# Performance work log

Hardware: AMD Instinct MI355X
Metric: run time of the kernel (lower is better)

The kernel has to match this reference:

```python
import jax, jax.numpy as jnp
import numpy as np

D_MODEL = 1024
NUM_HEADS = 16
HEAD_DIM = D_MODEL // NUM_HEADS


def setup_inputs() -> dict:
    key = jax.random.key(0)
    ks = jax.random.split(key, 5)
    s = 1.0 / np.sqrt(D_MODEL)
    return {
        "x": jax.random.normal(ks[0], (2, 2048, D_MODEL), dtype=jnp.float32),
        "Wqkv": jax.random.normal(ks[1], (3 * D_MODEL, D_MODEL), dtype=jnp.float32) * s,
        "bqkv": jax.random.normal(ks[2], (3 * D_MODEL,), dtype=jnp.float32) * s,
        "Wo": jax.random.normal(ks[3], (D_MODEL, D_MODEL), dtype=jnp.float32) * s,
        "bo": jax.random.normal(ks[4], (D_MODEL,), dtype=jnp.float32) * s,
    }


def reference(x, Wqkv, bqkv, Wo, bo):
    B, S, D = x.shape
    H, hd = NUM_HEADS, HEAD_DIM
    # fused QKV projection (torch Linear: x @ W.T + b)
    qkv = x @ Wqkv.T + bqkv                      # [B, S, 3D]
    qkv = qkv.reshape(B, S, H, 3 * hd).transpose(0, 2, 1, 3)  # [B, H, S, 3hd]
    q, k, v = jnp.split(qkv, 3, axis=-1)         # each [B, H, S, hd]
    scaled = jnp.einsum("bhqd,bhkd->bhqk", q, k) / jnp.sqrt(jnp.float32(hd))
    # module applies causal mask when its `mask` flag is False (the default)
    causal = jnp.tril(jnp.ones((S, S), dtype=bool))
    scaled = jnp.where(causal, scaled, -jnp.inf)
    attn = jax.nn.softmax(scaled, axis=-1)       # [B, H, S, S]
    values = jnp.einsum("bhqk,bhkd->bhqd", attn, v)  # [B, H, S, hd]
    # NOTE: original uses .reshape (not transpose-then-reshape) on the
    # [B, H, S, hd] tensor directly — reproduce that exact layout.
    values = values.reshape(B, S, H * hd)
    out = values @ Wo.T + bo                     # [B, S, D]
    return out
```

## Files before the change

### kernel.cpp

```cpp
#include <hip/hip_runtime.h>

typedef __attribute__((ext_vector_type(8))) short bf16x8;
typedef __attribute__((ext_vector_type(4))) float f32x4;

#define D_MODEL 1024
#define NHEADS 16
#define HDIM 64
#define SEQ 2048
#define BATCH 2
#define MROWS (BATCH*SEQ)
#define NQKV (3*D_MODEL)
#define QSCALE 0.1803368801111204f
#define CSTR 144

__device__ __forceinline__ unsigned short f2bf(float f) {
  unsigned int u = __float_as_uint(f);
  u += 0x7FFF + ((u >> 16) & 1);
  return (unsigned short)(u >> 16);
}
__device__ __forceinline__ unsigned int pack2bf(float a, float b) {
#if __has_builtin(__builtin_amdgcn_cvt_pk_bf16_f32)
  auto r = __builtin_amdgcn_cvt_pk_bf16_f32(a, b);
  unsigned int u; __builtin_memcpy(&u, &r, 4);
  return u;
#else
  return ((unsigned int)f2bf(b) << 16) | (unsigned int)f2bf(a);
#endif
}

__device__ __forceinline__ void gload16(const void* g, void* l) {
  __builtin_amdgcn_global_load_lds((const __attribute__((address_space(1))) void*)g,
                                   (__attribute__((address_space(3))) void*)l, 16, 0, 0);
}

#define N4_X     1048576
#define N4_WQKV   786432
#define N4_WO     262144
__global__ void cvt_all_kernel(const float4* __restrict__ x,
                               const float4* __restrict__ wqkv,
                               const float4* __restrict__ wo,
                               ushort4* __restrict__ xb,
                               ushort4* __restrict__ wqkvb,
                               ushort4* __restrict__ wob) {
  int i = blockIdx.x * blockDim.x + threadIdx.x;
  const float4* s; ushort4* d; int j;
  if (i < N4_X)                { s = x;    d = xb;    j = i; }
  else if (i < N4_X + N4_WQKV) { s = wqkv; d = wqkvb; j = i - N4_X; }
  else                         { s = wo;   d = wob;   j = i - (N4_X + N4_WQKV); }
  float4 v = s[j];
  ushort4 o;
  o.x = f2bf(v.x); o.y = f2bf(v.y); o.z = f2bf(v.z); o.w = f2bf(v.w);
  d[j] = o;
}

template<int MODE, int BM>
__global__ __launch_bounds__(256) void gemm_bt_kernel(
    const unsigned short* __restrict__ A,
    const unsigned short* __restrict__ Bm,
    const float* __restrict__ bias,
    float* __restrict__ outF,
    unsigned short* __restrict__ Qb,
    unsigned short* __restrict__ Kb,
    unsigned short* __restrict__ VTb,
    int M, int N, int K)
{
  constexpr int MI = BM / 32;
  constexpr int STG = BM*32 + 128*32;
  constexpr int SHSZ = (MODE == 0 && 128*CSTR > 2*STG) ? 128*CSTR : 2*STG;
  __shared__ __align__(16) unsigned short Sh[SHSZ];
  const int tid = threadIdx.x;
  const int wave = tid >> 6, lane = tid & 63;
  const int lm = lane & 15, quad = lane >> 4;
  const int wm = (wave >> 1) * (BM/2), wn = (wave & 1) * 64;
  const int m0 = blockIdx.y * BM, n0 = blockIdx.x * 128;

  f32x4 acc[MI][4] = {};

  auto stage_in = [&](int k0, int sb) {
    unsigned short* As = Sh + sb*STG;
    unsigned short* Bs = As + BM*32;
#pragma unroll
    for (int i = 0; i < BM/64; i++) {
      int ch = i*256 + tid;
      int r = ch >> 2, cg = (ch & 3) ^ ((r >> 1) & 3);
      gload16(&A[(size_t)(m0 + r) * K + k0 + cg*8], &As[ch*8]);
    }
#pragma unroll
    for (int i = 0; i < 2; i++) {
      int ch = i*256 + tid;
      int r = ch >> 2, cg = (ch & 3) ^ ((r >> 1) & 3);
      gload16(&Bm[(size_t)(n0 + r) * K + k0 + cg*8], &Bs[ch*8]);
    }
  };

  stage_in(0, 0);
  for (int k0 = 0; k0 < K; k0 += 32) {
    const int cur = (k0 >> 5) & 1;
    __syncthreads();
    if (k0 + 32 < K) stage_in(k0 + 32, cur ^ 1);
    const unsigned short* As = Sh + cur*STG;
    const unsigned short* Bs = As + BM*32;
    bf16x8 af[MI], bfr[4];
#pragma unroll
    for (int mi = 0; mi < MI; mi++) {
      int r = wm + mi*16 + lm;
      af[mi] = *(const bf16x8*)&As[(r*4 + (quad ^ ((r >> 1) & 3))) * 8];
    }
#pragma unroll
    for (int ni = 0; ni < 4; ni++) {
      int r = wn + ni*16 + lm;
      bfr[ni] = *(const bf16x8*)&Bs[(r*4 + (quad ^ ((r >> 1) & 3))) * 8];
    }
#pragma unroll
    for (int mi = 0; mi < MI; mi++)
#pragma unroll
      for (int ni = 0; ni < 4; ni++)
        acc[mi][ni] = __builtin_amdgcn_mfma_f32_16x16x32_bf16(af[mi], bfr[ni], acc[mi][ni], 0, 0, 0);
  }

  if (MODE == 1) {
#pragma unroll
    for (int mi = 0; mi < MI; mi++)
#pragma unroll
      for (int ni = 0; ni < 4; ni++)
#pragma unroll
        for (int r = 0; r < 4; r++) {
          int row = m0 + wm + mi*16 + quad*4 + r;
          int col = n0 + wn + ni*16 + lm;
          outF[(size_t)row * N + col] = acc[mi][ni][r] + bias[col];
        }
  } else {
    __syncthreads();
#pragma unroll
    for (int mi = 0; mi < MI; mi++)
#pragma unroll
      for (int ni = 0; ni < 4; ni++)
#pragma unroll
        for (int r = 0; r < 4; r++) {
          int row_l = wm + mi*16 + quad*4 + r;
          int col_l = wn + ni*16 + lm;
          int col = n0 + col_l;
          float v = acc[mi][ni][r] + bias[col];
          if (((col % 192) >> 6) == 0) v *= QSCALE;
          Sh[row_l*CSTR + col_l] = f2bf(v);
        }
    __syncthreads();
#pragma unroll
    for (int i = 0; i < 8; i++) {
      int lin = i*256 + tid;
      int row_l = lin >> 4, cc = (lin & 15) * 8;
      int col = n0 + cc;
      int h = col / 192, rr = col - h*192;
      int ty = rr >> 6, e = rr & 63;
      if (ty < 2) {
        uint4 d = *(const uint4*)&Sh[row_l*CSTR + cc];
        int row = m0 + row_l;
        int b = row >> 11, s = row & (SEQ - 1);
        unsigned short* dst = ty ? Kb : Qb;
        *(uint4*)&dst[((size_t)(b*NHEADS + h)*SEQ + s)*HDIM + e] = d;
      }
    }
#pragma unroll
    for (int i = 0; i < 8; i++) {
      int lin = i*256 + tid;
      int col_l = lin & 127, s8 = (lin >> 7) * 8;
      int col = n0 + col_l;
      int h = col / 192, rr = col - h*192;
      if ((rr >> 6) == 2) {
        int e = rr & 63;
        unsigned short tmp[8];
#pragma unroll
        for (int j = 0; j < 8; j++) tmp[j] = Sh[(s8 + j)*CSTR + col_l];
        int row = m0 + s8;
        int b = row >> 11, s = row & (SEQ - 1);
        size_t vb = ((size_t)(b*NHEADS + h)*HDIM + e)*SEQ;
        int pos = (s & ~31) | (((s >> 2) & 3) << 3) | (((s >> 4) & 1) << 2);
        *(uint2*)&VTb[vb + pos]     = *(const uint2*)&tmp[0];
        *(uint2*)&VTb[vb + pos + 8] = *(const uint2*)&tmp[4];
      }
    }
  }
}

__global__ __launch_bounds__(256) void flash_attn_kernel(
    const unsigned short* __restrict__ Qb,
    const unsigned short* __restrict__ Kb,
    const unsigned short* __restrict__ VTb,
    unsigned short* __restrict__ Ob)
{
  const int tid = threadIdx.x;
  const int wave = tid >> 6, lane = tid & 63;
  const int lm = lane & 15, quad = lane >> 4;
  const int bx = blockIdx.x;
  const int bh = (bx & 7) * 4 + (bx >> 3);
  const int pr = blockIdx.y;
  const int t0 = 31 - pr, t1 = pr;
  const int nk0 = (t0 + 2) >> 1;
  const int ntot = nk0 + ((t1 + 2) >> 1);

  __shared__ __align__(16) unsigned short Ks[2][128*64];
  __shared__ __align__(16) unsigned short Vs[2][64*128];

  const unsigned short* Qbh  = Qb  + (size_t)bh*SEQ*HDIM;
  const unsigned short* Kbh  = Kb  + (size_t)bh*SEQ*HDIM;
  const unsigned short* VTbh = VTb + (size_t)bh*HDIM*SEQ;

  auto stage_in = [&](int k0, int sb) {
#pragma unroll
    for (int i = 0; i < 4; i++) {
      int ch = i*256 + tid;
      int r = ch >> 3, cg = (ch & 7) ^ (r & 7);
      gload16(&Kbh[(size_t)(k0 + r)*HDIM + cg*8], &Ks[sb][ch*8]);
    }
#pragma unroll
    for (int i = 0; i < 4; i++) {
      int ch = i*256 + tid;
      int e = ch >> 4, cg = (ch & 15) ^ (e & 7);
      gload16(&VTbh[(size_t)e*SEQ + k0 + cg*8], &Vs[sb][ch*8]);
    }
  };

  int rowq = t0*64 + wave*16;
  int query = rowq + lm;
  bf16x8 qf[2];
#pragma unroll
  for (int kc = 0; kc < 2; kc++)
    qf[kc] = *(const bf16x8*)&Qbh[(size_t)query*HDIM + kc*32 + quad*8];

  f32x4 o[4] = {};
  float m_run = -1e30f, l_run = 0.f;

  stage_in(0, 0);
  for (int s = 0; s < ntot; s++) {
    const int kt = (s < nk0) ? s : s - nk0;
    const int k0 = kt * 128;
    const int cur = s & 1;
    __syncthreads();
    if (s + 1 < ntot) {
      int sn = s + 1;
      int ktn = (sn < nk0) ? sn : sn - nk0;
      stage_in(ktn * 128, cur ^ 1);
    }

    f32x4 sc[8] = {};
#pragma unroll
    for (int kc = 0; kc < 2; kc++)
#pragma unroll
      for (int mi = 0; mi < 8; mi++) {
        int r = mi*16 + lm, cc = kc*4 + quad;
        bf16x8 kf = *(const bf16x8*)&Ks[cur][(r*8 + (cc ^ (r & 7))) * 8];
        sc[mi] = __builtin_amdgcn_mfma_f32_16x16x32_bf16(kf, qf[kc], sc[mi], 0, 0, 0);
      }

    if (k0 + 127 > rowq) {
#pragma unroll
      for (int mi = 0; mi < 8; mi++)
#pragma unroll
        for (int r = 0; r < 4; r++) {
          int key = k0 + mi*16 + quad*4 + r;
          if (key > query) sc[mi][r] = -1e30f;
        }
    }

    float tr[8];
#pragma unroll
    for (int mi = 0; mi < 8; mi++)
      tr[mi] = fmaxf(fmaxf(sc[mi][0], sc[mi][1]), fmaxf(sc[mi][2], sc[mi][3]));
#pragma unroll
    for (int st = 4; st > 0; st >>= 1)
#pragma unroll
      for (int j = 0; j < st; j++) tr[j] = fmaxf(tr[j], tr[j + st]);
    float mx = tr[0];
    mx = fmaxf(mx, __shfl_xor(mx, 16, 64));
    mx = fmaxf(mx, __shfl_xor(mx, 32, 64));
    float mnew = fmaxf(m_run, mx);
    float alpha = exp2f(m_run - mnew);
    float p[8][4];
#pragma unroll
    for (int mi = 0; mi < 8; mi++)
#pragma unroll
      for (int r = 0; r < 4; r++)
        p[mi][r] = exp2f(sc[mi][r] - mnew);
    float sr[8];
#pragma unroll
    for (int mi = 0; mi < 8; mi++)
      sr[mi] = (p[mi][0] + p[mi][1]) + (p[mi][2] + p[mi][3]);
#pragma unroll
    for (int st = 4; st > 0; st >>= 1)
#pragma unroll
      for (int j = 0; j < st; j++) sr[j] += sr[j + st];
    float rs = sr[0];
    rs += __shfl_xor(rs, 16, 64);
    rs += __shfl_xor(rs, 32, 64);
    l_run = l_run * alpha + rs;
    if (__any(mnew != m_run)) {
#pragma unroll
      for (int ei = 0; ei < 4; ei++)
#pragma unroll
        for (int r = 0; r < 4; r++) o[ei][r] *= alpha;
    }
    m_run = mnew;

#pragma unroll
    for (int kc = 0; kc < 4; kc++) {
      union { unsigned int w[4]; bf16x8 v; } pu;
      pu.w[0] = pack2bf(p[2*kc][0],   p[2*kc][1]);
      pu.w[1] = pack2bf(p[2*kc][2],   p[2*kc][3]);
      pu.w[2] = pack2bf(p[2*kc+1][0], p[2*kc+1][1]);
      pu.w[3] = pack2bf(p[2*kc+1][2], p[2*kc+1][3]);
#pragma unroll
      for (int ei = 0; ei < 4; ei++) {
        int e = ei*16 + lm, cc = kc*4 + quad;
        bf16x8 vf = *(const bf16x8*)&Vs[cur][(e*16 + (cc ^ (e & 7))) * 8];
        o[ei] = __builtin_amdgcn_mfma_f32_16x16x32_bf16(vf, pu.v, o[ei], 0, 0, 0);
      }
    }

    if (s == nk0 - 1 || s == ntot - 1) {
      float inv = 1.0f / l_run;
      size_t obase = ((size_t)bh*SEQ + query) * HDIM;
#pragma unroll
      for (int ei = 0; ei < 4; ei++) {
        uint2 u;
        u.x = pack2bf(o[ei][0]*inv, o[ei][1]*inv);
        u.y = pack2bf(o[ei][2]*inv, o[ei][3]*inv);
        *(uint2*)&Ob[obase + ei*16 + quad*4] = u;
      }
      if (s == nk0 - 1) {
        rowq = t1*64 + wave*16;
        query = rowq + lm;
#pragma unroll
        for (int kc = 0; kc < 2; kc++)
          qf[kc] = *(const bf16x8*)&Qbh[(size_t)query*HDIM + kc*32 + quad*8];
#pragma unroll
        for (int ei = 0; ei < 4; ei++)
#pragma unroll
          for (int r = 0; r < 4; r++) o[ei][r] = 0.f;
        m_run = -1e30f; l_run = 0.f;
      }
    }
  }
}

extern "C" void kernel_launch(void* const* d_in, const int* in_sizes, int n_in,
                              void* d_out, int out_size, void* d_ws, size_t ws_size,
                              hipStream_t stream) {
  const float* x    = (const float*)d_in[0];
  const float* Wqkv = (const float*)d_in[1];
  const float* bqkv = (const float*)d_in[2];
  const float* Wo   = (const float*)d_in[3];
  const float* bo   = (const float*)d_in[4];
  float* out = (float*)d_out;

  char* ws = (char*)d_ws;
  unsigned short* Xbf    = (unsigned short*)(ws);
  unsigned short* Wqkvbf = (unsigned short*)(ws + 8388608);
  unsigned short* Wobf   = (unsigned short*)(ws + 14680064);
  unsigned short* Qb     = (unsigned short*)(ws + 16777216);
  unsigned short* Kb     = (unsigned short*)(ws + 25165824);
  unsigned short* VTb    = (unsigned short*)(ws + 33554432);
  unsigned short* Ob     = (unsigned short*)(ws + 41943040);

  cvt_all_kernel<<<8192, 256, 0, stream>>>(
      (const float4*)x, (const float4*)Wqkv, (const float4*)Wo,
      (ushort4*)Xbf, (ushort4*)Wqkvbf, (ushort4*)Wobf);

  gemm_bt_kernel<0,128><<<dim3(24, 32), 256, 0, stream>>>(
      Xbf, Wqkvbf, bqkv, nullptr, Qb, Kb, VTb, MROWS, NQKV, D_MODEL);

  flash_attn_kernel<<<dim3(32, 16), 256, 0, stream>>>(Qb, Kb, VTb, Ob);

  gemm_bt_kernel<1,64><<<dim3(8, 64), 256, 0, stream>>>(
      Ob, Wobf, bo, out, nullptr, nullptr, nullptr, MROWS, D_MODEL, D_MODEL);
}
```

Before: 188.1 us.

## Double query rows per wave in flash attention to reuse K/V tiles

Each wave now handles two 16-row query groups (128 query rows per block instead of 64), so every K and V fragment read from shared memory feeds two MFMAs, and the grid is halved. Causal pairing of tiles is adjusted to 16 tile pairs, launch bounds request 2 blocks per SIMD/CU, and s_setprio raises wave priority around MFMA sections. The aim is to cut LDS traffic and loop overhead per unit of work. The cost is higher register pressure from doubled accumulators and score arrays, and fewer blocks to spread across CUs.

Result: slower. 197.8 us (+5.2%).

```diff
diff --git a/kernel.cpp b/kernel.cpp
--- a/kernel.cpp
+++ b/kernel.cpp
@@ -182,7 +182,7 @@
   }
 }
 
-__global__ __launch_bounds__(256) void flash_attn_kernel(
+__global__ __launch_bounds__(256, 2) void flash_attn_kernel(
     const unsigned short* __restrict__ Qb,
     const unsigned short* __restrict__ Kb,
     const unsigned short* __restrict__ VTb,
@@ -194,9 +194,9 @@
   const int bx = blockIdx.x;
   const int bh = (bx & 7) * 4 + (bx >> 3);
   const int pr = blockIdx.y;
-  const int t0 = 31 - pr, t1 = pr;
-  const int nk0 = (t0 + 2) >> 1;
-  const int ntot = nk0 + ((t1 + 2) >> 1);
+  const int t0 = 15 - pr, t1 = pr;
+  const int nk0 = t0 + 1;
+  const int ntot = nk0 + t1 + 1;
 
   __shared__ __align__(16) unsigned short Ks[2][128*64];
   __shared__ __align__(16) unsigned short Vs[2][64*128];
@@ -220,15 +220,19 @@
     }
   };
 
-  int rowq = t0*64 + wave*16;
-  int query = rowq + lm;
-  bf16x8 qf[2];
-#pragma unroll
-  for (int kc = 0; kc < 2; kc++)
-    qf[kc] = *(const bf16x8*)&Qbh[(size_t)query*HDIM + kc*32 + quad*8];
-
-  f32x4 o[4] = {};
-  float m_run = -1e30f, l_run = 0.f;
+  int rowq = t0*128 + wave*32;
+  int query[2];
+  bf16x8 qf[2][2];
+#pragma unroll
+  for (int g = 0; g < 2; g++) {
+    query[g] = rowq + g*16 + lm;
+#pragma unroll
+    for (int kc = 0; kc < 2; kc++)
+      qf[g][kc] = *(const bf16x8*)&Qbh[(size_t)query[g]*HDIM + kc*32 + quad*8];
+  }
+
+  f32x4 o[2][4] = {};
+  float m_run[2] = {-1e30f, -1e30f}, l_run[2] = {0.f, 0.f};
 
   stage_in(0, 0);
   for (int s = 0; s < ntot; s++) {
@@ -242,101 +246,122 @@
       stage_in(ktn * 128, cur ^ 1);
     }
 
-    f32x4 sc[8] = {};
+    f32x4 sc[2][8] = {};
+    __builtin_amdgcn_s_setprio(1);
 #pragma unroll
     for (int kc = 0; kc < 2; kc++)
 #pragma unroll
       for (int mi = 0; mi < 8; mi++) {
         int r = mi*16 + lm, cc = kc*4 + quad;
         bf16x8 kf = *(const bf16x8*)&Ks[cur][(r*8 + (cc ^ (r & 7))) * 8];
-        sc[mi] = __builtin_amdgcn_mfma_f32_16x16x32_bf16(kf, qf[kc], sc[mi], 0, 0, 0);
-      }
+        sc[0][mi] = __builtin_amdgcn_mfma_f32_16x16x32_bf16(kf, qf[0][kc], sc[0][mi], 0, 0, 0);
+        sc[1][mi] = __builtin_amdgcn_mfma_f32_16x16x32_bf16(kf, qf[1][kc], sc[1][mi], 0, 0, 0);
+      }
+    __builtin_amdgcn_s_setprio(0);
 
     if (k0 + 127 > rowq) {
 #pragma unroll
+      for (int g = 0; g < 2; g++)
+#pragma unroll
+        for (int mi = 0; mi < 8; mi++)
+#pragma unroll
+          for (int r = 0; r < 4; r++) {
+            int key = k0 + mi*16 + quad*4 + r;
+            if (key > query[g]) sc[g][mi][r] = -1e30f;
+          }
+    }
+
+    bf16x8 pf[2][4];
+#pragma unroll
+    for (int g = 0; g < 2; g++) {
+      float tr8[8];
+#pragma unroll
       for (int mi = 0; mi < 8; mi++)
-#pragma unroll
-        for (int r = 0; r < 4; r++) {
-          int key = k0 + mi*16 + quad*4 + r;
-          if (key > query) sc[mi][r] = -1e30f;
-        }
-    }
-
-    float tr[8];
-#pragma unroll
-    for (int mi = 0; mi < 8; mi++)
-      tr[mi] = fmaxf(fmaxf(sc[mi][0], sc[mi][1]), fmaxf(sc[mi][2], sc[mi][3]));
-#pragma unroll
-    for (int st = 4; st > 0; st >>= 1)
-#pragma unroll
-      for (int j = 0; j < st; j++) tr[j] = fmaxf(tr[j], tr[j + st]);
-    float mx = tr[0];
-    mx = fmaxf(mx, __shfl_xor(mx, 16, 64));
-    mx = fmaxf(mx, __shfl_xor(mx, 32, 64));
-    float mnew = fmaxf(m_run, mx);
-    float alpha = exp2f(m_run - mnew);
-    float p[8][4];
-#pragma unroll
-    for (int mi = 0; mi < 8; mi++)
-#pragma unroll
-      for (int r = 0; r < 4; r++)
-        p[mi][r] = exp2f(sc[mi][r] - mnew);
-    float sr[8];
-#pragma unroll
-    for (int mi = 0; mi < 8; mi++)
-      sr[mi] = (p[mi][0] + p[mi][1]) + (p[mi][2] + p[mi][3]);
-#pragma unroll
-    for (int st = 4; st > 0; st >>= 1)
-#pragma unroll
-      for (int j = 0; j < st; j++) sr[j] += sr[j + st];
-    float rs = sr[0];
-    rs += __shfl_xor(rs, 16, 64);
-    rs += __shfl_xor(rs, 32, 64);
-    l_run = l_run * alpha + rs;
-    if (__any(mnew != m_run)) {
-#pragma unroll
-      for (int ei = 0; ei < 4; ei++)
-#pragma unroll
-        for (int r = 0; r < 4; r++) o[ei][r] *= alpha;
-    }
-    m_run = mnew;
-
-#pragma unroll
-    for (int kc = 0; kc < 4; kc++) {
-      union { unsigned int w[4]; bf16x8 v; } pu;
-      pu.w[0] = pack2bf(p[2*kc][0],   p[2*kc][1]);
-      pu.w[1] = pack2bf(p[2*kc][2],   p[2*kc][3]);
-      pu.w[2] = pack2bf(p[2*kc+1][0], p[2*kc+1][1]);
-      pu.w[3] = pack2bf(p[2*kc+1][2], p[2*kc+1][3]);
+        tr8[mi] = fmaxf(fmaxf(sc[g][mi][0], sc[g][mi][1]), fmaxf(sc[g][mi][2], sc[g][mi][3]));
+#pragma unroll
+      for (int st = 4; st > 0; st >>= 1)
+#pragma unroll
+        for (int j = 0; j < st; j++) tr8[j] = fmaxf(tr8[j], tr8[j + st]);
+      float mx = tr8[0];
+      mx = fmaxf(mx, __shfl_xor(mx, 16, 64));
+      mx = fmaxf(mx, __shfl_xor(mx, 32, 64));
+      float mnew = fmaxf(m_run[g], mx);
+      float alpha = exp2f(m_run[g] - mnew);
+      float p[8][4];
+#pragma unroll
+      for (int mi = 0; mi < 8; mi++)
+#pragma unroll
+        for (int r2 = 0; r2 < 4; r2++)
+          p[mi][r2] = exp2f(sc[g][mi][r2] - mnew);
+      float sr8[8];
+#pragma unroll
+      for (int mi = 0; mi < 8; mi++)
+        sr8[mi] = (p[mi][0] + p[mi][1]) + (p[mi][2] + p[mi][3]);
+#pragma unroll
+      for (int st = 4; st > 0; st >>= 1)
+#pragma unroll
+        for (int j = 0; j < st; j++) sr8[j] += sr8[j + st];
+      float rs = sr8[0];
+      rs += __shfl_xor(rs, 16, 64);
+      rs += __shfl_xor(rs, 32, 64);
+      l_run[g] = l_run[g] * alpha + rs;
+      if (__any(mnew != m_run[g])) {
+#pragma unroll
+        for (int ei = 0; ei < 4; ei++)
+#pragma unroll
+          for (int r2 = 0; r2 < 4; r2++) o[g][ei][r2] *= alpha;
+      }
+      m_run[g] = mnew;
+#pragma unroll
+      for (int kc = 0; kc < 4; kc++) {
+        union { unsigned int w[4]; bf16x8 v; } pu;
+        pu.w[0] = pack2bf(p[2*kc][0],   p[2*kc][1]);
+        pu.w[1] = pack2bf(p[2*kc][2],   p[2*kc][3]);
+        pu.w[2] = pack2bf(p[2*kc+1][0], p[2*kc+1][1]);
+        pu.w[3] = pack2bf(p[2*kc+1][2], p[2*kc+1][3]);
+        pf[g][kc] = pu.v;
+      }
+    }
+
+    __builtin_amdgcn_s_setprio(1);
+#pragma unroll
+    for (int kc = 0; kc < 4; kc++)
 #pragma unroll
       for (int ei = 0; ei < 4; ei++) {
         int e = ei*16 + lm, cc = kc*4 + quad;
         bf16x8 vf = *(const bf16x8*)&Vs[cur][(e*16 + (cc ^ (e & 7))) * 8];
-        o[ei] = __builtin_amdgcn_mfma_f32_16x16x32_bf16(vf, pu.v, o[ei], 0, 0, 0);
-      }
-    }
+        o[0][ei] = __builtin_amdgcn_mfma_f32_16x16x32_bf16(vf, pf[0][kc], o[0][ei], 0, 0, 0);
+        o[1][ei] = __builtin_amdgcn_mfma_f32_16x16x32_bf16(vf, pf[1][kc], o[1][ei], 0, 0, 0);
+      }
+    __builtin_amdgcn_s_setprio(0);
 
     if (s == nk0 - 1 || s == ntot - 1) {
-      float inv = 1.0f / l_run;
-      size_t obase = ((size_t)bh*SEQ + query) * HDIM;
-#pragma unroll
-      for (int ei = 0; ei < 4; ei++) {
-        uint2 u;
-        u.x = pack2bf(o[ei][0]*inv, o[ei][1]*inv);
-        u.y = pack2bf(o[ei][2]*inv, o[ei][3]*inv);
-        *(uint2*)&Ob[obase + ei*16 + quad*4] = u;
+#pragma unroll
+      for (int g = 0; g < 2; g++) {
+        float inv = 1.0f / l_run[g];
+        size_t obase = ((size_t)bh*SEQ + query[g]) * HDIM;
+#pragma unroll
+        for (int ei = 0; ei < 4; ei++) {
+          uint2 u;
+          u.x = pack2bf(o[g][ei][0]*inv, o[g][ei][1]*inv);
+          u.y = pack2bf(o[g][ei][2]*inv, o[g][ei][3]*inv);
+          *(uint2*)&Ob[obase + ei*16 + quad*4] = u;
+        }
       }
       if (s == nk0 - 1) {
-        rowq = t1*64 + wave*16;
-        query = rowq + lm;
-#pragma unroll
-        for (int kc = 0; kc < 2; kc++)
-          qf[kc] = *(const bf16x8*)&Qbh[(size_t)query*HDIM + kc*32 + quad*8];
-#pragma unroll
-        for (int ei = 0; ei < 4; ei++)
-#pragma unroll
-          for (int r = 0; r < 4; r++) o[ei][r] = 0.f;
-        m_run = -1e30f; l_run = 0.f;
+        rowq = t1*128 + wave*32;
+#pragma unroll
+        for (int g = 0; g < 2; g++) {
+          query[g] = rowq + g*16 + lm;
+#pragma unroll
+          for (int kc = 0; kc < 2; kc++)
+            qf[g][kc] = *(const bf16x8*)&Qbh[(size_t)query[g]*HDIM + kc*32 + quad*8];
+#pragma unroll
+          for (int ei = 0; ei < 4; ei++)
+#pragma unroll
+            for (int r2 = 0; r2 < 4; r2++) o[g][ei][r2] = 0.f;
+          m_run[g] = -1e30f; l_run[g] = 0.f;
+        }
       }
     }
   }
@@ -368,7 +393,7 @@
   gemm_bt_kernel<0,128><<<dim3(24, 32), 256, 0, stream>>>(
       Xbf, Wqkvbf, bqkv, nullptr, Qb, Kb, VTb, MROWS, NQKV, D_MODEL);
 
-  flash_attn_kernel<<<dim3(32, 16), 256, 0, stream>>>(Qb, Kb, VTb, Ob);
+  flash_attn_kernel<<<dim3(32, 8), 256, 0, stream>>>(Qb, Kb, VTb, Ob);
 
   gemm_bt_kernel<1,64><<<dim3(8, 64), 256, 0, stream>>>(
       Ob, Wobf, bo, out, nullptr, nullptr, nullptr, MROWS, D_MODEL, D_MODEL);
```
